# Optimization experiments

Hardware: AMD Instinct MI355X
Metric: run time of the kernel (lower is better)

Reference implementation:

```python
import jax, jax.numpy as jnp
import numpy as np


def setup_inputs() -> dict:
    key = jax.random.key(0)
    k1, k2, k3 = jax.random.split(key, 3)
    B, C, H, W = 64, 1024, 32, 32
    x = jax.random.normal(k1, (B, C, H, W), dtype=jnp.float32)
    # Conv2d(C, 1, kernel_size=1): weight [1, C, 1, 1] -> flatten to [C], bias [1] -> scalar
    bound = 1.0 / np.sqrt(C)
    attn_w = jax.random.uniform(k2, (C,), dtype=jnp.float32, minval=-bound, maxval=bound)
    attn_b = jax.random.uniform(k3, (), dtype=jnp.float32, minval=-bound, maxval=bound)
    return {"x": x, "attn_w": attn_w, "attn_b": attn_b}


def reference(x, attn_w, attn_b):
    B, C, H, W = x.shape
    # 1x1 conv producing one channel: score[b,h,w] = sum_c x[b,c,h,w]*w[c] + b
    scores = jnp.einsum('bchw,c->bhw', x, attn_w) + attn_b          # [B,H,W]
    attn = jax.nn.softmax(scores.reshape(B, -1), axis=-1)           # softmax over H*W
    attn = attn.reshape(B, H, W)
    # weighted sum pooling over spatial dims
    out = jnp.einsum('bchw,bhw->bc', x, attn)                       # [B,C]
    return out
```

## Files before the change

### kernel.cpp

```cpp
#include <hip/hip_runtime.h>

#define NB 64
#define NC 1024
#define NHW 1024
#define THW 16
#define NT (NHW / THW)

__global__ __launch_bounds__(256) void fused_partial_kernel(
        const float* __restrict__ x, const float* __restrict__ w,
        float* __restrict__ partial, float* __restrict__ mz) {
    __shared__ float red[4][THW];
    __shared__ float pbuf[THW];

    const int tid  = threadIdx.x;
    const int wave = tid >> 6, lane = tid & 63;
    const int bid  = blockIdx.x;
    const int b    = bid >> 6;
    const int hw0  = (bid & 63) * THW;
    const int cg   = tid >> 2;
    const int m    = lane & 3;

    const float* base = x + ((size_t)(b * NC + cg)) * NHW + hw0 + m * 4;
    float4 xv[16];
    float  wj[16];
    #pragma unroll
    for (int i = 0; i < 16; ++i) {
        xv[i] = *reinterpret_cast<const float4*>(base + (size_t)i * 64 * NHW);
        wj[i] = w[cg + (i << 6)];
    }

    float sp[4] = {0.f, 0.f, 0.f, 0.f};
    #pragma unroll
    for (int i = 0; i < 16; ++i) {
        sp[0] += xv[i].x * wj[i];
        sp[1] += xv[i].y * wj[i];
        sp[2] += xv[i].z * wj[i];
        sp[3] += xv[i].w * wj[i];
    }
    #pragma unroll
    for (int k = 0; k < 4; ++k) {
        #pragma unroll
        for (int off = 4; off < 64; off <<= 1)
            sp[k] += __shfl_xor(sp[k], off);
    }
    if (lane < 4) {
        #pragma unroll
        for (int k = 0; k < 4; ++k) red[wave][lane * 4 + k] = sp[k];
    }
    __syncthreads();

    if (tid < THW) {
        float s = red[0][tid] + red[1][tid] + red[2][tid] + red[3][tid];
        float mx = s;
        #pragma unroll
        for (int off = 8; off; off >>= 1) mx = fmaxf(mx, __shfl_xor(mx, off, 16));
        float e = __expf(s - mx);
        float z = e;
        #pragma unroll
        for (int off = 8; off; off >>= 1) z += __shfl_xor(z, off, 16);
        pbuf[tid] = e;
        if (tid == 0) {
            mz[2 * bid]     = mx;
            mz[2 * bid + 1] = z;
        }
    }
    __syncthreads();

    const float4 ev = *reinterpret_cast<const float4*>(&pbuf[m * 4]);
    #pragma unroll
    for (int i = 0; i < 16; ++i) {
        float t = xv[i].x * ev.x + xv[i].y * ev.y + xv[i].z * ev.z + xv[i].w * ev.w;
        t += __shfl_xor(t, 1);
        t += __shfl_xor(t, 2);
        if ((i & 3) == m)
            partial[(size_t)bid * NC + (i << 6) + cg] = t;
    }
}

__global__ __launch_bounds__(256) void combine_kernel(
        const float* __restrict__ partial, const float* __restrict__ mz,
        float* __restrict__ out) {
    __shared__ float scale[NT];
    const int tid = threadIdx.x;
    const int b   = blockIdx.x >> 2;
    const int c   = ((blockIdx.x & 3) << 8) + tid;

    if (tid < NT) {
        const float m_t = mz[2 * (b * NT + tid)];
        const float Z_t = mz[2 * (b * NT + tid) + 1];
        float mg = m_t;
        #pragma unroll
        for (int off = 32; off; off >>= 1) mg = fmaxf(mg, __shfl_xor(mg, off));
        const float ew = __expf(m_t - mg);
        float z = Z_t * ew;
        #pragma unroll
        for (int off = 32; off; off >>= 1) z += __shfl_xor(z, off);
        scale[tid] = ew / z;
    }
    __syncthreads();

    float acc = 0.0f;
    const float* p = partial + (size_t)b * NT * NC + c;
    #pragma unroll 8
    for (int t = 0; t < NT; ++t)
        acc += p[(size_t)t * NC] * scale[t];
    out[b * NC + c] = acc;
}

extern "C" void kernel_launch(void* const* d_in, const int* in_sizes, int n_in,
                              void* d_out, int out_size, void* d_ws, size_t ws_size,
                              hipStream_t stream) {
    const float* x = (const float*)d_in[0];
    const float* w = (const float*)d_in[1];
    float* out     = (float*)d_out;
    float* partial = (float*)d_ws;
    float* mz      = partial + (size_t)NB * NT * NC;

    fused_partial_kernel<<<NB * NT, 256, 0, stream>>>(x, w, partial, mz);
    combine_kernel<<<NB * (NC / 256), 256, 0, stream>>>(partial, mz, out);
}
```

Baseline: 98.86 us.

## Widen spatial tile to 64 with 512-thread blocks and LDS-staged weights and partials

The spatial tile grows from 16 to 64 positions per block, and blocks grow to 512 threads, each holding 32 float4 values in registers. Weights are staged once in LDS, and each 16-lane group reads 64 contiguous floats per channel row, giving wider coalesced loads. Pooled partials are staged in LDS and written as float2. The partial buffer and the combine kernel's reduction shrink from 64 to 16 tiles per batch. The risks are high register pressure (128 registers per thread for x under a launch bound of 512 with min 8), a longer shuffle reduction, and fewer blocks in the grid.

Result: slower. 136.8 us (+38.4%).

```diff
diff --git a/kernel.cpp b/kernel.cpp
--- a/kernel.cpp
+++ b/kernel.cpp
@@ -3,78 +3,82 @@
 #define NB 64
 #define NC 1024
 #define NHW 1024
-#define THW 16
+#define THW 64
 #define NT (NHW / THW)
 
-__global__ __launch_bounds__(256) void fused_partial_kernel(
+__global__ __launch_bounds__(512, 8) void tile_kernel(
         const float* __restrict__ x, const float* __restrict__ w,
         float* __restrict__ partial, float* __restrict__ mz) {
-    __shared__ float red[4][THW];
-    __shared__ float pbuf[THW];
+    __shared__ float w_lds[NC];
+    __shared__ float scr[8][THW];
+    __shared__ float e_lds[THW];
+    __shared__ float pool_lds[NC];
 
     const int tid  = threadIdx.x;
-    const int wave = tid >> 6, lane = tid & 63;
+    const int lane = tid & 63;
+    const int wv   = tid >> 6;
+    const int g    = tid & 15;
+    const int rp   = tid >> 4;
     const int bid  = blockIdx.x;
-    const int b    = bid >> 6;
-    const int hw0  = (bid & 63) * THW;
-    const int cg   = tid >> 2;
-    const int m    = lane & 3;
+    const int b    = bid >> 4;
+    const int hw0  = (bid & 15) * THW;
 
-    const float* base = x + ((size_t)(b * NC + cg)) * NHW + hw0 + m * 4;
-    float4 xv[16];
-    float  wj[16];
-    #pragma unroll
-    for (int i = 0; i < 16; ++i) {
-        xv[i] = *reinterpret_cast<const float4*>(base + (size_t)i * 64 * NHW);
-        wj[i] = w[cg + (i << 6)];
-    }
+    if (tid < NC / 4)
+        reinterpret_cast<float4*>(w_lds)[tid] =
+            reinterpret_cast<const float4*>(w)[tid];
+    __syncthreads();
 
+    const float* xb = x + ((size_t)b * NC) * NHW + hw0 + g * 4;
+    float4 v[32];
     float sp[4] = {0.f, 0.f, 0.f, 0.f};
     #pragma unroll
-    for (int i = 0; i < 16; ++i) {
-        sp[0] += xv[i].x * wj[i];
-        sp[1] += xv[i].y * wj[i];
-        sp[2] += xv[i].z * wj[i];
-        sp[3] += xv[i].w * wj[i];
+    for (int i = 0; i < 32; ++i) {
+        const int row = i * 32 + rp;
+        v[i] = *reinterpret_cast<const float4*>(xb + (size_t)row * NHW);
+        const float wr = w_lds[row];
+        sp[0] += v[i].x * wr;  sp[1] += v[i].y * wr;
+        sp[2] += v[i].z * wr;  sp[3] += v[i].w * wr;
     }
     #pragma unroll
     for (int k = 0; k < 4; ++k) {
+        sp[k] += __shfl_xor(sp[k], 16);
+        sp[k] += __shfl_xor(sp[k], 32);
+    }
+    if (lane < 16)
+        *reinterpret_cast<float4*>(&scr[wv][lane * 4]) =
+            make_float4(sp[0], sp[1], sp[2], sp[3]);
+    __syncthreads();
+
+    if (tid < THW) {
+        float s = 0.f;
         #pragma unroll
-        for (int off = 4; off < 64; off <<= 1)
-            sp[k] += __shfl_xor(sp[k], off);
-    }
-    if (lane < 4) {
+        for (int k = 0; k < 8; ++k) s += scr[k][tid];
+        float m = s;
         #pragma unroll
-        for (int k = 0; k < 4; ++k) red[wave][lane * 4 + k] = sp[k];
+        for (int off = 32; off; off >>= 1) m = fmaxf(m, __shfl_xor(m, off));
+        float e = __expf(s - m);
+        float z = e;
+        #pragma unroll
+        for (int off = 32; off; off >>= 1) z += __shfl_xor(z, off);
+        e_lds[tid] = e;
+        if (tid == 0) { mz[2 * bid] = m; mz[2 * bid + 1] = z; }
     }
     __syncthreads();
 
-    if (tid < THW) {
-        float s = red[0][tid] + red[1][tid] + red[2][tid] + red[3][tid];
-        float mx = s;
-        #pragma unroll
-        for (int off = 8; off; off >>= 1) mx = fmaxf(mx, __shfl_xor(mx, off, 16));
-        float e = __expf(s - mx);
-        float z = e;
-        #pragma unroll
-        for (int off = 8; off; off >>= 1) z += __shfl_xor(z, off, 16);
-        pbuf[tid] = e;
-        if (tid == 0) {
-            mz[2 * bid]     = mx;
-            mz[2 * bid + 1] = z;
-        }
+    const float4 ev = *reinterpret_cast<const float4*>(&e_lds[g * 4]);
+    #pragma unroll
+    for (int i = 0; i < 32; ++i) {
+        float t = v[i].x * ev.x + v[i].y * ev.y + v[i].z * ev.z + v[i].w * ev.w;
+        t += __shfl_xor(t, 1);
+        t += __shfl_xor(t, 2);
+        t += __shfl_xor(t, 4);
+        t += __shfl_xor(t, 8);
+        if (g == 0) pool_lds[i * 32 + rp] = t;
     }
     __syncthreads();
 
-    const float4 ev = *reinterpret_cast<const float4*>(&pbuf[m * 4]);
-    #pragma unroll
-    for (int i = 0; i < 16; ++i) {
-        float t = xv[i].x * ev.x + xv[i].y * ev.y + xv[i].z * ev.z + xv[i].w * ev.w;
-        t += __shfl_xor(t, 1);
-        t += __shfl_xor(t, 2);
-        if ((i & 3) == m)
-            partial[(size_t)bid * NC + (i << 6) + cg] = t;
-    }
+    reinterpret_cast<float2*>(partial + (size_t)bid * NC)[tid] =
+        reinterpret_cast<const float2*>(pool_lds)[tid];
 }
 
 __global__ __launch_bounds__(256) void combine_kernel(
@@ -87,21 +91,21 @@
 
     if (tid < NT) {
         const float m_t = mz[2 * (b * NT + tid)];
-        const float Z_t = mz[2 * (b * NT + tid) + 1];
-        float mg = m_t;
+        const float z_t = mz[2 * (b * NT + tid) + 1];
+        float M = m_t;
         #pragma unroll
-        for (int off = 32; off; off >>= 1) mg = fmaxf(mg, __shfl_xor(mg, off));
-        const float ew = __expf(m_t - mg);
-        float z = Z_t * ew;
+        for (int off = 8; off; off >>= 1) M = fmaxf(M, __shfl_xor(M, off, 16));
+        const float ew = __expf(m_t - M);
+        float Z = z_t * ew;
         #pragma unroll
-        for (int off = 32; off; off >>= 1) z += __shfl_xor(z, off);
-        scale[tid] = ew / z;
+        for (int off = 8; off; off >>= 1) Z += __shfl_xor(Z, off, 16);
+        scale[tid] = ew / Z;
     }
     __syncthreads();
 
-    float acc = 0.0f;
+    float acc = 0.f;
     const float* p = partial + (size_t)b * NT * NC + c;
-    #pragma unroll 8
+    #pragma unroll
     for (int t = 0; t < NT; ++t)
         acc += p[(size_t)t * NC] * scale[t];
     out[b * NC + c] = acc;
@@ -116,6 +120,6 @@
     float* partial = (float*)d_ws;
     float* mz      = partial + (size_t)NB * NT * NC;
 
-    fused_partial_kernel<<<NB * NT, 256, 0, stream>>>(x, w, partial, mz);
-    combine_kernel<<<NB * (NC / 256), 256, 0, stream>>>(partial, mz, out);
+    tile_kernel<<<NB * NT, 512, 0, stream>>>(x, w, partial, mz);
+    combine_kernel<<<NB * 4, 256, 0, stream>>>(partial, mz, out);
 }
```
